# Performance work log

Hardware: AMD Instinct MI355X
Metric: run time of the kernel (lower is better)

## Reference

```python
import jax, jax.numpy as jnp
import numpy as np

N_NODES = 500000
N_EDGES = 600000
N_GRAPHS = 1024
D = 128        # node/edge/global feature dim
IN_DIM = 3 * D # 384
OUT_DIM = 128


def setup_inputs() -> dict:
    key = jax.random.key(0)
    k1, k2, k3, k4, k5, k6, k7 = jax.random.split(key, 7)
    x = jax.random.normal(k1, (N_NODES, D), dtype=jnp.float32)
    edge_index = jax.random.randint(k2, (2, N_EDGES), 0, N_NODES, dtype=jnp.int64)
    edge_attr = jax.random.normal(k3, (N_EDGES, D), dtype=jnp.float32)
    u = jax.random.normal(k4, (N_GRAPHS, D), dtype=jnp.float32)
    batch = jnp.sort(jax.random.randint(k5, (N_NODES,), 0, N_GRAPHS, dtype=jnp.int64))
    # Linear(in_dim, out_dim) params, torch default init scale
    lim = 1.0 / np.sqrt(IN_DIM)
    W = jax.random.uniform(k6, (OUT_DIM, IN_DIM), minval=-lim, maxval=lim, dtype=jnp.float32)
    b = jax.random.uniform(k7, (OUT_DIM,), minval=-lim, maxval=lim, dtype=jnp.float32)
    return {"x": x, "edge_index": edge_index, "edge_attr": edge_attr,
            "u": u, "batch": batch, "W": W, "b": b}


def reference(x, edge_index, edge_attr, u, batch, W, b):
    num_graphs = u.shape[0]
    # scatter(x, batch, reduce='sum') -> [G, d_node]
    node_agg = jax.ops.segment_sum(x, batch, num_segments=num_graphs)
    # scatter(edge_attr, batch[edge_index[0]], reduce='sum') -> [G, d_edge]
    edge_seg = batch[edge_index[0]]
    edge_agg = jax.ops.segment_sum(edge_attr, edge_seg, num_segments=num_graphs)
    inp = jnp.concatenate([node_agg, edge_agg, u], axis=-1)  # [G, in_dim]
    out = jax.nn.relu(inp @ W.T + b)                         # [G, out_dim]
    return out
```

## Files before the change

kernel.cpp:

```cpp
#include <hip/hip_runtime.h>

constexpr int kNodes  = 500000;
constexpr int kEdges  = 600000;
constexpr int kGraphs = 1024;
constexpr int kD      = 128;
constexpr int kNP     = 16;
constexpr int kBins   = kGraphs * kNP;
constexpr int kEPB    = 1024;
constexpr int kHistBlocks = (kEdges + kEPB - 1) / kEPB;

constexpr size_t kAccNOff  = 0;
constexpr size_t kAccEOff  = 1u << 20;
constexpr size_t kOrderOff = 2u << 20;
constexpr size_t kCntOff   = (2u << 20) + 2400000;
constexpr size_t kOffsOff  = kCntOff + 65536;
constexpr size_t kCursOff  = kOffsOff + 65536;

__global__ __launch_bounds__(256) void hist_kernel(
    const int* __restrict__ ei0, const int* __restrict__ batch,
    int* __restrict__ counts) {
  const int b = blockIdx.x;
  const int base = b * kEPB + threadIdx.x * 4;
  int* cp = counts + (b & (kNP - 1));
  if (base + 3 < kEdges) {
    const int4 e = *reinterpret_cast<const int4*>(ei0 + base);
    atomicAdd(cp + batch[e.x] * kNP, 1);
    atomicAdd(cp + batch[e.y] * kNP, 1);
    atomicAdd(cp + batch[e.z] * kNP, 1);
    atomicAdd(cp + batch[e.w] * kNP, 1);
  } else {
    for (int j = 0; j < 4; ++j) {
      const int r = base + j;
      if (r < kEdges) atomicAdd(cp + batch[ei0[r]] * kNP, 1);
    }
  }
}

__global__ __launch_bounds__(1024) void scan_kernel(
    const int* __restrict__ counts, int* __restrict__ offs,
    int* __restrict__ curs) {
  __shared__ int s[1024];
  const int t = threadIdx.x;
  int v[16];
  int tot = 0;
#pragma unroll
  for (int k = 0; k < 16; ++k) {
    v[k] = counts[t * 16 + k];
    tot += v[k];
  }
  s[t] = tot;
  __syncthreads();
  for (int off = 1; off < 1024; off <<= 1) {
    const int add = (t >= off) ? s[t - off] : 0;
    __syncthreads();
    s[t] += add;
    __syncthreads();
  }
  int run = s[t] - tot;
#pragma unroll
  for (int k = 0; k < 16; ++k) {
    offs[t * 16 + k] = run;
    curs[t * 16 + k] = run;
    run += v[k];
  }
}

__global__ __launch_bounds__(256) void scatter_kernel(
    const int* __restrict__ ei0, const int* __restrict__ batch,
    int* __restrict__ curs, int* __restrict__ order) {
  const int b = blockIdx.x;
  const int base = b * kEPB + threadIdx.x * 4;
  int* cp = curs + (b & (kNP - 1));
  if (base + 3 < kEdges) {
    const int4 e = *reinterpret_cast<const int4*>(ei0 + base);
    const int p0 = atomicAdd(cp + batch[e.x] * kNP, 1);
    const int p1 = atomicAdd(cp + batch[e.y] * kNP, 1);
    const int p2 = atomicAdd(cp + batch[e.z] * kNP, 1);
    const int p3 = atomicAdd(cp + batch[e.w] * kNP, 1);
    order[p0] = base;
    order[p1] = base + 1;
    order[p2] = base + 2;
    order[p3] = base + 3;
  } else {
    for (int j = 0; j < 4; ++j) {
      const int r = base + j;
      if (r < kEdges) {
        const int pos = atomicAdd(cp + batch[ei0[r]] * kNP, 1);
        order[pos] = r;
      }
    }
  }
}

__global__ __launch_bounds__(256) void node_sum_kernel(
    const float* __restrict__ x, const int* __restrict__ batch,
    float* __restrict__ accN) {
  __shared__ int s_b[2];
  __shared__ float s_red[8][128];
  const int tid = threadIdx.x;
  const int sub = tid & 31, rlane = tid >> 5;
  const int g = blockIdx.x >> 1, h = blockIdx.x & 1;

  if (tid < 2) {
    const int target = g + tid;
    int lo = 0, hi = kNodes;
    while (lo < hi) {
      const int mid = (lo + hi) >> 1;
      if (batch[mid] < target) lo = mid + 1; else hi = mid;
    }
    s_b[tid] = lo;
  }
  __syncthreads();
  const int s = s_b[0], e = s_b[1];
  const int mid = (s + e) >> 1;
  const int s0 = h ? mid : s, e0 = h ? e : mid;

  float4 a0 = make_float4(0.f, 0.f, 0.f, 0.f);
  float4 a1 = a0, a2 = a0, a3 = a0;
  const float4* rows = reinterpret_cast<const float4*>(x);
  int r = s0 + rlane;
  for (; r + 24 < e0; r += 32) {
    const float4 v0 = rows[(size_t)r * 32 + sub];
    const float4 v1 = rows[(size_t)(r + 8) * 32 + sub];
    const float4 v2 = rows[(size_t)(r + 16) * 32 + sub];
    const float4 v3 = rows[(size_t)(r + 24) * 32 + sub];
    a0.x += v0.x; a0.y += v0.y; a0.z += v0.z; a0.w += v0.w;
    a1.x += v1.x; a1.y += v1.y; a1.z += v1.z; a1.w += v1.w;
    a2.x += v2.x; a2.y += v2.y; a2.z += v2.z; a2.w += v2.w;
    a3.x += v3.x; a3.y += v3.y; a3.z += v3.z; a3.w += v3.w;
  }
  for (; r < e0; r += 8) {
    const float4 v = rows[(size_t)r * 32 + sub];
    a0.x += v.x; a0.y += v.y; a0.z += v.z; a0.w += v.w;
  }

  a0.x += a1.x + a2.x + a3.x;
  a0.y += a1.y + a2.y + a3.y;
  a0.z += a1.z + a2.z + a3.z;
  a0.w += a1.w + a2.w + a3.w;
  s_red[rlane][sub * 4 + 0] = a0.x;
  s_red[rlane][sub * 4 + 1] = a0.y;
  s_red[rlane][sub * 4 + 2] = a0.z;
  s_red[rlane][sub * 4 + 3] = a0.w;
  __syncthreads();
  if (tid < kD) {
    float sm = 0.f;
#pragma unroll
    for (int k = 0; k < 8; ++k) sm += s_red[k][tid];
    accN[((size_t)h * kGraphs + g) * kD + tid] = sm;
  }
}

__global__ __launch_bounds__(256) void edge_sum_kernel(
    const float* __restrict__ edge_attr, const int* __restrict__ order,
    const int* __restrict__ offs, float* __restrict__ accE) {
  __shared__ int s_b[2];
  __shared__ int s_idx[1024];
  __shared__ float s_red[8][128];
  const int tid = threadIdx.x;
  const int sub = tid & 31, rlane = tid >> 5;
  const int g = blockIdx.x >> 1, h = blockIdx.x & 1;

  if (tid == 0) {
    const int s = offs[g * kNP];
    const int e = (g == kGraphs - 1) ? kEdges : offs[(g + 1) * kNP];
    const int mid = (s + e) >> 1;
    s_b[0] = h ? mid : s;
    s_b[1] = h ? e : mid;
  }
  __syncthreads();
  const int s = s_b[0], e = s_b[1];

  float4 a0 = make_float4(0.f, 0.f, 0.f, 0.f);
  float4 a1 = a0, a2 = a0, a3 = a0;
  const float4* rows = reinterpret_cast<const float4*>(edge_attr);
  for (int t0 = s; t0 < e; t0 += 1024) {
    const int n = min(1024, e - t0);
    __syncthreads();
    for (int i = tid; i < n; i += 256) s_idx[i] = order[t0 + i];
    __syncthreads();
    int i = rlane;
    for (; i + 24 < n; i += 32) {
      const int i0 = s_idx[i], i1 = s_idx[i + 8];
      const int i2 = s_idx[i + 16], i3 = s_idx[i + 24];
      const float4 v0 = rows[(size_t)i0 * 32 + sub];
      const float4 v1 = rows[(size_t)i1 * 32 + sub];
      const float4 v2 = rows[(size_t)i2 * 32 + sub];
      const float4 v3 = rows[(size_t)i3 * 32 + sub];
      a0.x += v0.x; a0.y += v0.y; a0.z += v0.z; a0.w += v0.w;
      a1.x += v1.x; a1.y += v1.y; a1.z += v1.z; a1.w += v1.w;
      a2.x += v2.x; a2.y += v2.y; a2.z += v2.z; a2.w += v2.w;
      a3.x += v3.x; a3.y += v3.y; a3.z += v3.z; a3.w += v3.w;
    }
    for (; i < n; i += 8) {
      const float4 v = rows[(size_t)s_idx[i] * 32 + sub];
      a0.x += v.x; a0.y += v.y; a0.z += v.z; a0.w += v.w;
    }
  }

  a0.x += a1.x + a2.x + a3.x;
  a0.y += a1.y + a2.y + a3.y;
  a0.z += a1.z + a2.z + a3.z;
  a0.w += a1.w + a2.w + a3.w;
  s_red[rlane][sub * 4 + 0] = a0.x;
  s_red[rlane][sub * 4 + 1] = a0.y;
  s_red[rlane][sub * 4 + 2] = a0.z;
  s_red[rlane][sub * 4 + 3] = a0.w;
  __syncthreads();
  if (tid < kD) {
    float sm = 0.f;
#pragma unroll
    for (int k = 0; k < 8; ++k) sm += s_red[k][tid];
    accE[((size_t)h * kGraphs + g) * kD + tid] = sm;
  }
}

__global__ __launch_bounds__(128) void fused_out_kernel(
    const float* __restrict__ accN, const float* __restrict__ accE,
    const float* __restrict__ u, const float* __restrict__ W,
    const float* __restrict__ b, float* __restrict__ out) {
  __shared__ float s_in[384];
  const int g = blockIdx.x;
  const int j = threadIdx.x;
  constexpr size_t kHalf = (size_t)kGraphs * kD;

  s_in[j]       = accN[(size_t)g * kD + j] + accN[kHalf + (size_t)g * kD + j];
  s_in[128 + j] = accE[(size_t)g * kD + j] + accE[kHalf + (size_t)g * kD + j];
  s_in[256 + j] = u[(size_t)g * kD + j];
  __syncthreads();

  float sum = b[j];
  const float4* Wr = reinterpret_cast<const float4*>(W + (size_t)j * 384);
  const float4* Sr = reinterpret_cast<const float4*>(s_in);
#pragma unroll 8
  for (int k = 0; k < 96; ++k) {
    const float4 w = Wr[k];
    const float4 s = Sr[k];
    sum = fmaf(w.x, s.x, sum);
    sum = fmaf(w.y, s.y, sum);
    sum = fmaf(w.z, s.z, sum);
    sum = fmaf(w.w, s.w, sum);
  }
  out[(size_t)g * kD + j] = fmaxf(sum, 0.f);
}

extern "C" void kernel_launch(void* const* d_in, const int* in_sizes, int n_in,
                              void* d_out, int out_size, void* d_ws,
                              size_t ws_size, hipStream_t stream) {
  const float* x         = (const float*)d_in[0];
  const int*   edge_idx  = (const int*)d_in[1];
  const float* edge_attr = (const float*)d_in[2];
  const float* u         = (const float*)d_in[3];
  const int*   batch     = (const int*)d_in[4];
  const float* W         = (const float*)d_in[5];
  const float* b         = (const float*)d_in[6];
  float*       out       = (float*)d_out;

  char* ws = (char*)d_ws;
  float* accN   = (float*)(ws + kAccNOff);
  float* accE   = (float*)(ws + kAccEOff);
  int*   order  = (int*)(ws + kOrderOff);
  int*   counts = (int*)(ws + kCntOff);
  int*   offs   = (int*)(ws + kOffsOff);
  int*   curs   = (int*)(ws + kCursOff);

  hipMemsetAsync(counts, 0, kBins * sizeof(int), stream);

  hist_kernel<<<kHistBlocks, 256, 0, stream>>>(edge_idx, batch, counts);
  scan_kernel<<<1, 1024, 0, stream>>>(counts, offs, curs);
  scatter_kernel<<<kHistBlocks, 256, 0, stream>>>(edge_idx, batch, curs, order);
  node_sum_kernel<<<2 * kGraphs, 256, 0, stream>>>(x, batch, accN);
  edge_sum_kernel<<<2 * kGraphs, 256, 0, stream>>>(edge_attr, order, offs,
                                                   accE);
  fused_out_kernel<<<kGraphs, 128, 0, stream>>>(accN, accE, u, W, b, out);
}
```

Measured before the change: 665.4 us.

## Fuse all stages into one cooperative kernel with grid-wide syncs

```diff
diff --git a/kernel.cpp b/kernel.cpp
--- a/kernel.cpp
+++ b/kernel.cpp
@@ -1,4 +1,7 @@
 #include <hip/hip_runtime.h>
+#include <hip/hip_cooperative_groups.h>
+
+namespace cg = cooperative_groups;
 
 constexpr int kNodes  = 500000;
 constexpr int kEdges  = 600000;
@@ -6,103 +9,35 @@
 constexpr int kD      = 128;
 constexpr int kNP     = 16;
 constexpr int kBins   = kGraphs * kNP;
-constexpr int kEPB    = 1024;
-constexpr int kHistBlocks = (kEdges + kEPB - 1) / kEPB;
-
-constexpr size_t kAccNOff  = 0;
-constexpr size_t kAccEOff  = 1u << 20;
-constexpr size_t kOrderOff = 2u << 20;
-constexpr size_t kCntOff   = (2u << 20) + 2400000;
-constexpr size_t kOffsOff  = kCntOff + 65536;
-constexpr size_t kCursOff  = kOffsOff + 65536;
-
-__global__ __launch_bounds__(256) void hist_kernel(
-    const int* __restrict__ ei0, const int* __restrict__ batch,
-    int* __restrict__ counts) {
-  const int b = blockIdx.x;
-  const int base = b * kEPB + threadIdx.x * 4;
-  int* cp = counts + (b & (kNP - 1));
-  if (base + 3 < kEdges) {
-    const int4 e = *reinterpret_cast<const int4*>(ei0 + base);
-    atomicAdd(cp + batch[e.x] * kNP, 1);
-    atomicAdd(cp + batch[e.y] * kNP, 1);
-    atomicAdd(cp + batch[e.z] * kNP, 1);
-    atomicAdd(cp + batch[e.w] * kNP, 1);
-  } else {
-    for (int j = 0; j < 4; ++j) {
-      const int r = base + j;
-      if (r < kEdges) atomicAdd(cp + batch[ei0[r]] * kNP, 1);
-    }
-  }
-}
-
-__global__ __launch_bounds__(1024) void scan_kernel(
-    const int* __restrict__ counts, int* __restrict__ offs,
-    int* __restrict__ curs) {
-  __shared__ int s[1024];
-  const int t = threadIdx.x;
-  int v[16];
-  int tot = 0;
-#pragma unroll
-  for (int k = 0; k < 16; ++k) {
-    v[k] = counts[t * 16 + k];
-    tot += v[k];
-  }
-  s[t] = tot;
-  __syncthreads();
-  for (int off = 1; off < 1024; off <<= 1) {
-    const int add = (t >= off) ? s[t - off] : 0;
-    __syncthreads();
-    s[t] += add;
-    __syncthreads();
-  }
-  int run = s[t] - tot;
-#pragma unroll
-  for (int k = 0; k < 16; ++k) {
-    offs[t * 16 + k] = run;
-    curs[t * 16 + k] = run;
-    run += v[k];
-  }
-}
-
-__global__ __launch_bounds__(256) void scatter_kernel(
-    const int* __restrict__ ei0, const int* __restrict__ batch,
-    int* __restrict__ curs, int* __restrict__ order) {
-  const int b = blockIdx.x;
-  const int base = b * kEPB + threadIdx.x * 4;
-  int* cp = curs + (b & (kNP - 1));
-  if (base + 3 < kEdges) {
-    const int4 e = *reinterpret_cast<const int4*>(ei0 + base);
-    const int p0 = atomicAdd(cp + batch[e.x] * kNP, 1);
-    const int p1 = atomicAdd(cp + batch[e.y] * kNP, 1);
-    const int p2 = atomicAdd(cp + batch[e.z] * kNP, 1);
-    const int p3 = atomicAdd(cp + batch[e.w] * kNP, 1);
-    order[p0] = base;
-    order[p1] = base + 1;
-    order[p2] = base + 2;
-    order[p3] = base + 3;
-  } else {
-    for (int j = 0; j < 4; ++j) {
-      const int r = base + j;
-      if (r < kEdges) {
-        const int pos = atomicAdd(cp + batch[ei0[r]] * kNP, 1);
-        order[pos] = r;
-      }
-    }
-  }
-}
-
-__global__ __launch_bounds__(256) void node_sum_kernel(
-    const float* __restrict__ x, const int* __restrict__ batch,
-    float* __restrict__ accN) {
-  __shared__ int s_b[2];
+constexpr int kChunk  = 588;
+
+constexpr size_t kOrderOff = 0;
+constexpr size_t kCntOff   = 2400000;
+constexpr size_t kOffsOff  = kCntOff + kBins * 4;
+constexpr size_t kCursOff  = kOffsOff + kBins * 4;
+
+__global__ __launch_bounds__(256, 4) void mega_kernel(
+    const float* __restrict__ x, const int* __restrict__ ei0,
+    const float* __restrict__ edge_attr, const float* __restrict__ u,
+    const int* __restrict__ batch, const float* __restrict__ W,
+    const float* __restrict__ bias, float* __restrict__ out,
+    int* __restrict__ order, int* __restrict__ counts,
+    int* __restrict__ offs, int* __restrict__ curs) {
+  cg::grid_group grid = cg::this_grid();
+  const int tid  = threadIdx.x;
+  const int blk  = blockIdx.x;
+  const int sub  = tid & 31;
+  const int rlane = tid >> 5;
+
+  __shared__ int   s_b[2];
+  __shared__ int   s_idx[1024];
   __shared__ float s_red[8][128];
-  const int tid = threadIdx.x;
-  const int sub = tid & 31, rlane = tid >> 5;
-  const int g = blockIdx.x >> 1, h = blockIdx.x & 1;
-
+  __shared__ int   s_scan[256];
+  __shared__ float s_in[384];
+
+  if (tid < kNP) counts[blk * kNP + tid] = 0;
   if (tid < 2) {
-    const int target = g + tid;
+    const int target = blk + tid;
     int lo = 0, hi = kNodes;
     while (lo < hi) {
       const int mid = (lo + hi) >> 1;
@@ -111,166 +46,192 @@
     s_b[tid] = lo;
   }
   __syncthreads();
-  const int s = s_b[0], e = s_b[1];
-  const int mid = (s + e) >> 1;
-  const int s0 = h ? mid : s, e0 = h ? e : mid;
-
-  float4 a0 = make_float4(0.f, 0.f, 0.f, 0.f);
-  float4 a1 = a0, a2 = a0, a3 = a0;
-  const float4* rows = reinterpret_cast<const float4*>(x);
-  int r = s0 + rlane;
-  for (; r + 24 < e0; r += 32) {
-    const float4 v0 = rows[(size_t)r * 32 + sub];
-    const float4 v1 = rows[(size_t)(r + 8) * 32 + sub];
-    const float4 v2 = rows[(size_t)(r + 16) * 32 + sub];
-    const float4 v3 = rows[(size_t)(r + 24) * 32 + sub];
-    a0.x += v0.x; a0.y += v0.y; a0.z += v0.z; a0.w += v0.w;
-    a1.x += v1.x; a1.y += v1.y; a1.z += v1.z; a1.w += v1.w;
-    a2.x += v2.x; a2.y += v2.y; a2.z += v2.z; a2.w += v2.w;
-    a3.x += v3.x; a3.y += v3.y; a3.z += v3.z; a3.w += v3.w;
-  }
-  for (; r < e0; r += 8) {
-    const float4 v = rows[(size_t)r * 32 + sub];
-    a0.x += v.x; a0.y += v.y; a0.z += v.z; a0.w += v.w;
-  }
-
-  a0.x += a1.x + a2.x + a3.x;
-  a0.y += a1.y + a2.y + a3.y;
-  a0.z += a1.z + a2.z + a3.z;
-  a0.w += a1.w + a2.w + a3.w;
-  s_red[rlane][sub * 4 + 0] = a0.x;
-  s_red[rlane][sub * 4 + 1] = a0.y;
-  s_red[rlane][sub * 4 + 2] = a0.z;
-  s_red[rlane][sub * 4 + 3] = a0.w;
-  __syncthreads();
-  if (tid < kD) {
-    float sm = 0.f;
-#pragma unroll
-    for (int k = 0; k < 8; ++k) sm += s_red[k][tid];
-    accN[((size_t)h * kGraphs + g) * kD + tid] = sm;
-  }
-}
-
-__global__ __launch_bounds__(256) void edge_sum_kernel(
-    const float* __restrict__ edge_attr, const int* __restrict__ order,
-    const int* __restrict__ offs, float* __restrict__ accE) {
-  __shared__ int s_b[2];
-  __shared__ int s_idx[1024];
-  __shared__ float s_red[8][128];
-  const int tid = threadIdx.x;
-  const int sub = tid & 31, rlane = tid >> 5;
-  const int g = blockIdx.x >> 1, h = blockIdx.x & 1;
-
-  if (tid == 0) {
-    const int s = offs[g * kNP];
-    const int e = (g == kGraphs - 1) ? kEdges : offs[(g + 1) * kNP];
-    const int mid = (s + e) >> 1;
-    s_b[0] = h ? mid : s;
-    s_b[1] = h ? e : mid;
-  }
-  __syncthreads();
-  const int s = s_b[0], e = s_b[1];
-
-  float4 a0 = make_float4(0.f, 0.f, 0.f, 0.f);
-  float4 a1 = a0, a2 = a0, a3 = a0;
-  const float4* rows = reinterpret_cast<const float4*>(edge_attr);
-  for (int t0 = s; t0 < e; t0 += 1024) {
-    const int n = min(1024, e - t0);
-    __syncthreads();
-    for (int i = tid; i < n; i += 256) s_idx[i] = order[t0 + i];
-    __syncthreads();
-    int i = rlane;
-    for (; i + 24 < n; i += 32) {
-      const int i0 = s_idx[i], i1 = s_idx[i + 8];
-      const int i2 = s_idx[i + 16], i3 = s_idx[i + 24];
-      const float4 v0 = rows[(size_t)i0 * 32 + sub];
-      const float4 v1 = rows[(size_t)i1 * 32 + sub];
-      const float4 v2 = rows[(size_t)i2 * 32 + sub];
-      const float4 v3 = rows[(size_t)i3 * 32 + sub];
+  const int nStart = s_b[0], nEnd = s_b[1];
+  grid.sync();
+
+  {
+    const int r = blk * kChunk + tid * 4;
+    if (tid * 4 < kChunk && r + 3 < kEdges) {
+      const int4 e4 = *reinterpret_cast<const int4*>(ei0 + r);
+      int* cp = counts + (blk & (kNP - 1));
+      atomicAdd(cp + batch[e4.x] * kNP, 1);
+      atomicAdd(cp + batch[e4.y] * kNP, 1);
+      atomicAdd(cp + batch[e4.z] * kNP, 1);
+      atomicAdd(cp + batch[e4.w] * kNP, 1);
+    }
+  }
+
+  float nodeSum;
+  {
+    float4 a0 = make_float4(0.f, 0.f, 0.f, 0.f);
+    float4 a1 = a0, a2 = a0, a3 = a0;
+    const float4* rows = reinterpret_cast<const float4*>(x);
+    int r = nStart + rlane;
+    for (; r + 24 < nEnd; r += 32) {
+      const float4 v0 = rows[(size_t)r * 32 + sub];
+      const float4 v1 = rows[(size_t)(r + 8) * 32 + sub];
+      const float4 v2 = rows[(size_t)(r + 16) * 32 + sub];
+      const float4 v3 = rows[(size_t)(r + 24) * 32 + sub];
       a0.x += v0.x; a0.y += v0.y; a0.z += v0.z; a0.w += v0.w;
       a1.x += v1.x; a1.y += v1.y; a1.z += v1.z; a1.w += v1.w;
       a2.x += v2.x; a2.y += v2.y; a2.z += v2.z; a2.w += v2.w;
       a3.x += v3.x; a3.y += v3.y; a3.z += v3.z; a3.w += v3.w;
     }
-    for (; i < n; i += 8) {
-      const float4 v = rows[(size_t)s_idx[i] * 32 + sub];
+    for (; r < nEnd; r += 8) {
+      const float4 v = rows[(size_t)r * 32 + sub];
       a0.x += v.x; a0.y += v.y; a0.z += v.z; a0.w += v.w;
     }
-  }
-
-  a0.x += a1.x + a2.x + a3.x;
-  a0.y += a1.y + a2.y + a3.y;
-  a0.z += a1.z + a2.z + a3.z;
-  a0.w += a1.w + a2.w + a3.w;
-  s_red[rlane][sub * 4 + 0] = a0.x;
-  s_red[rlane][sub * 4 + 1] = a0.y;
-  s_red[rlane][sub * 4 + 2] = a0.z;
-  s_red[rlane][sub * 4 + 3] = a0.w;
+    a0.x += a1.x + a2.x + a3.x;
+    a0.y += a1.y + a2.y + a3.y;
+    a0.z += a1.z + a2.z + a3.z;
+    a0.w += a1.w + a2.w + a3.w;
+    s_red[rlane][sub * 4 + 0] = a0.x;
+    s_red[rlane][sub * 4 + 1] = a0.y;
+    s_red[rlane][sub * 4 + 2] = a0.z;
+    s_red[rlane][sub * 4 + 3] = a0.w;
+    __syncthreads();
+    float sm = 0.f;
+    if (tid < kD) {
+#pragma unroll
+      for (int k = 0; k < 8; ++k) sm += s_red[k][tid];
+    }
+    nodeSum = sm;
+  }
+  grid.sync();
+
+  if (blk == 0) {
+    const int b0 = tid * 64;
+    int tot = 0;
+    for (int k = 0; k < 64; ++k) tot += counts[b0 + k];
+    s_scan[tid] = tot;
+    __syncthreads();
+    for (int off = 1; off < 256; off <<= 1) {
+      const int add = (tid >= off) ? s_scan[tid - off] : 0;
+      __syncthreads();
+      s_scan[tid] += add;
+      __syncthreads();
+    }
+    int run = s_scan[tid] - tot;
+    for (int k = 0; k < 64; ++k) {
+      const int c = counts[b0 + k];
+      offs[b0 + k] = run;
+      curs[b0 + k] = run;
+      run += c;
+    }
+  }
+  grid.sync();
+
+  {
+    const int r = blk * kChunk + tid * 4;
+    if (tid * 4 < kChunk && r + 3 < kEdges) {
+      const int4 e4 = *reinterpret_cast<const int4*>(ei0 + r);
+      int* cp = curs + (blk & (kNP - 1));
+      const int p0 = atomicAdd(cp + batch[e4.x] * kNP, 1);
+      const int p1 = atomicAdd(cp + batch[e4.y] * kNP, 1);
+      const int p2 = atomicAdd(cp + batch[e4.z] * kNP, 1);
+      const int p3 = atomicAdd(cp + batch[e4.w] * kNP, 1);
+      order[p0] = r;
+      order[p1] = r + 1;
+      order[p2] = r + 2;
+      order[p3] = r + 3;
+    }
+  }
+  grid.sync();
+
+  float edgeSum;
+  {
+    const int s = offs[blk * kNP];
+    const int e = (blk == kGraphs - 1) ? kEdges : offs[(blk + 1) * kNP];
+    float4 a0 = make_float4(0.f, 0.f, 0.f, 0.f);
+    float4 a1 = a0, a2 = a0, a3 = a0;
+    const float4* rows = reinterpret_cast<const float4*>(edge_attr);
+    for (int t0 = s; t0 < e; t0 += 1024) {
+      const int n = min(1024, e - t0);
+      __syncthreads();
+      for (int i = tid; i < n; i += 256) s_idx[i] = order[t0 + i];
+      __syncthreads();
+      int i = rlane;
+      for (; i + 24 < n; i += 32) {
+        const int i0 = s_idx[i],      i1 = s_idx[i + 8];
+        const int i2 = s_idx[i + 16], i3 = s_idx[i + 24];
+        const float4 v0 = rows[(size_t)i0 * 32 + sub];
+        const float4 v1 = rows[(size_t)i1 * 32 + sub];
+        const float4 v2 = rows[(size_t)i2 * 32 + sub];
+        const float4 v3 = rows[(size_t)i3 * 32 + sub];
+        a0.x += v0.x; a0.y += v0.y; a0.z += v0.z; a0.w += v0.w;
+        a1.x += v1.x; a1.y += v1.y; a1.z += v1.z; a1.w += v1.w;
+        a2.x += v2.x; a2.y += v2.y; a2.z += v2.z; a2.w += v2.w;
+        a3.x += v3.x; a3.y += v3.y; a3.z += v3.z; a3.w += v3.w;
+      }
+      for (; i < n; i += 8) {
+        const float4 v = rows[(size_t)s_idx[i] * 32 + sub];
+        a0.x += v.x; a0.y += v.y; a0.z += v.z; a0.w += v.w;
+      }
+    }
+    a0.x += a1.x + a2.x + a3.x;
+    a0.y += a1.y + a2.y + a3.y;
+    a0.z += a1.z + a2.z + a3.z;
+    a0.w += a1.w + a2.w + a3.w;
+    __syncthreads();
+    s_red[rlane][sub * 4 + 0] = a0.x;
+    s_red[rlane][sub * 4 + 1] = a0.y;
+    s_red[rlane][sub * 4 + 2] = a0.z;
+    s_red[rlane][sub * 4 + 3] = a0.w;
+    __syncthreads();
+    float sm = 0.f;
+    if (tid < kD) {
+#pragma unroll
+      for (int k = 0; k < 8; ++k) sm += s_red[k][tid];
+    }
+    edgeSum = sm;
+  }
+  grid.sync();
+
+  if (tid < kD) {
+    s_in[tid]          = nodeSum;
+    s_in[kD + tid]     = edgeSum;
+    s_in[2 * kD + tid] = u[(size_t)blk * kD + tid];
+  }
   __syncthreads();
   if (tid < kD) {
-    float sm = 0.f;
-#pragma unroll
-    for (int k = 0; k < 8; ++k) sm += s_red[k][tid];
-    accE[((size_t)h * kGraphs + g) * kD + tid] = sm;
-  }
-}
-
-__global__ __launch_bounds__(128) void fused_out_kernel(
-    const float* __restrict__ accN, const float* __restrict__ accE,
-    const float* __restrict__ u, const float* __restrict__ W,
-    const float* __restrict__ b, float* __restrict__ out) {
-  __shared__ float s_in[384];
-  const int g = blockIdx.x;
-  const int j = threadIdx.x;
-  constexpr size_t kHalf = (size_t)kGraphs * kD;
-
-  s_in[j]       = accN[(size_t)g * kD + j] + accN[kHalf + (size_t)g * kD + j];
-  s_in[128 + j] = accE[(size_t)g * kD + j] + accE[kHalf + (size_t)g * kD + j];
-  s_in[256 + j] = u[(size_t)g * kD + j];
-  __syncthreads();
-
-  float sum = b[j];
-  const float4* Wr = reinterpret_cast<const float4*>(W + (size_t)j * 384);
-  const float4* Sr = reinterpret_cast<const float4*>(s_in);
+    float sum = bias[tid];
+    const float4* Wr = reinterpret_cast<const float4*>(W + (size_t)tid * 384);
+    const float4* Sr = reinterpret_cast<const float4*>(s_in);
 #pragma unroll 8
-  for (int k = 0; k < 96; ++k) {
-    const float4 w = Wr[k];
-    const float4 s = Sr[k];
-    sum = fmaf(w.x, s.x, sum);
-    sum = fmaf(w.y, s.y, sum);
-    sum = fmaf(w.z, s.z, sum);
-    sum = fmaf(w.w, s.w, sum);
-  }
-  out[(size_t)g * kD + j] = fmaxf(sum, 0.f);
+    for (int k = 0; k < 96; ++k) {
+      const float4 w = Wr[k];
+      const float4 s = Sr[k];
+      sum = fmaf(w.x, s.x, sum);
+      sum = fmaf(w.y, s.y, sum);
+      sum = fmaf(w.z, s.z, sum);
+      sum = fmaf(w.w, s.w, sum);
+    }
+    out[(size_t)blk * kD + tid] = fmaxf(sum, 0.f);
+  }
 }
 
 extern "C" void kernel_launch(void* const* d_in, const int* in_sizes, int n_in,
                               void* d_out, int out_size, void* d_ws,
                               size_t ws_size, hipStream_t stream) {
   const float* x         = (const float*)d_in[0];
-  const int*   edge_idx  = (const int*)d_in[1];
+  const int*   ei0       = (const int*)d_in[1];
   const float* edge_attr = (const float*)d_in[2];
   const float* u         = (const float*)d_in[3];
   const int*   batch     = (const int*)d_in[4];
   const float* W         = (const float*)d_in[5];
-  const float* b         = (const float*)d_in[6];
+  const float* bias      = (const float*)d_in[6];
   float*       out       = (float*)d_out;
 
   char* ws = (char*)d_ws;
-  float* accN   = (float*)(ws + kAccNOff);
-  float* accE   = (float*)(ws + kAccEOff);
-  int*   order  = (int*)(ws + kOrderOff);
-  int*   counts = (int*)(ws + kCntOff);
-  int*   offs   = (int*)(ws + kOffsOff);
-  int*   curs   = (int*)(ws + kCursOff);
-
-  hipMemsetAsync(counts, 0, kBins * sizeof(int), stream);
-
-  hist_kernel<<<kHistBlocks, 256, 0, stream>>>(edge_idx, batch, counts);
-  scan_kernel<<<1, 1024, 0, stream>>>(counts, offs, curs);
-  scatter_kernel<<<kHistBlocks, 256, 0, stream>>>(edge_idx, batch, curs, order);
-  node_sum_kernel<<<2 * kGraphs, 256, 0, stream>>>(x, batch, accN);
-  edge_sum_kernel<<<2 * kGraphs, 256, 0, stream>>>(edge_attr, order, offs,
-                                                   accE);
-  fused_out_kernel<<<kGraphs, 128, 0, stream>>>(accN, accE, u, W, b, out);
+  int* order  = (int*)(ws + kOrderOff);
+  int* counts = (int*)(ws + kCntOff);
+  int* offs   = (int*)(ws + kOffsOff);
+  int* curs   = (int*)(ws + kCursOff);
+
+  void* args[] = {(void*)&x,     (void*)&ei0,  (void*)&edge_attr,
+                  (void*)&u,     (void*)&batch, (void*)&W,
+                  (void*)&bias,  (void*)&out,   (void*)&order,
+                  (void*)&counts, (void*)&offs, (void*)&curs};
+  hipLaunchCooperativeKernel((void*)mega_kernel, dim3(kGraphs), dim3(256),
+                             args, 0, stream);
 }
```

New measurement: 1.179 ms. 1.77x slower.
